# Kernel tuning notes

Measured on AMD Instinct MI355X. Metric: run time of the kernel, lower is better.

## Reference

```python
import jax, jax.numpy as jnp
import numpy as np

N_T = 256
N_LAT = 1024
N_INN = 512
N_G = 512
N_MU = 64
N_NEU = 1024  # MLP hidden width (both MLP_p and MLP_m)
N_HID = 2     # hidden layers per MLP


def _linear(x, w, b=None):
    y = x @ w.T
    return y if b is None else y + b


def _mlp(x, in_w, in_b, h0_w, h0_b, h1_w, h1_b, out_w, out_b):
    f = jax.nn.leaky_relu(_linear(x, in_w, in_b))
    f = jax.nn.leaky_relu(_linear(f, h0_w, h0_b))
    f = jax.nn.leaky_relu(_linear(f, h1_w, h1_b))
    return _linear(f, out_w, out_b)


def setup_inputs() -> dict:
    key = jax.random.key(0)
    ks = jax.random.split(key, 24)

    def w(k, out_f, in_f):
        return jax.random.normal(k, (out_f, in_f), jnp.float32) / np.sqrt(in_f)

    def b(k, out_f):
        return jax.random.normal(k, (out_f,), jnp.float32) * 0.01

    return {
        "mu": jax.random.normal(ks[0], (N_MU,), jnp.float32),
        "z_0": jax.random.normal(ks[1], (N_LAT,), jnp.float32),
        # attention projections (no bias)
        "W1": w(ks[2], N_LAT, N_INN),
        "W2": w(ks[3], N_INN, N_LAT),
        "W3": w(ks[4], N_G, N_LAT),
        # MLP_p: N_MU -> N_NEU -> (x2) -> N_LAT
        "p_in_w": w(ks[5], N_NEU, N_MU), "p_in_b": b(ks[6], N_NEU),
        "p_h0_w": w(ks[7], N_NEU, N_NEU), "p_h0_b": b(ks[8], N_NEU),
        "p_h1_w": w(ks[9], N_NEU, N_NEU), "p_h1_b": b(ks[10], N_NEU),
        "p_out_w": w(ks[11], N_LAT, N_NEU), "p_out_b": b(ks[12], N_LAT),
        # MLP_m: N_G -> N_NEU -> (x2) -> N_LAT
        "m_in_w": w(ks[13], N_NEU, N_G), "m_in_b": b(ks[14], N_NEU),
        "m_h0_w": w(ks[15], N_NEU, N_NEU), "m_h0_b": b(ks[16], N_NEU),
        "m_h1_w": w(ks[17], N_NEU, N_NEU), "m_h1_b": b(ks[18], N_NEU),
        "m_out_w": w(ks[19], N_LAT, N_NEU), "m_out_b": b(ks[20], N_LAT),
    }


def reference(mu, z_0, W1, W2, W3,
              p_in_w, p_in_b, p_h0_w, p_h0_b, p_h1_w, p_h1_b, p_out_w, p_out_b,
              m_in_w, m_in_b, m_h0_w, m_h0_b, m_h1_w, m_h1_b, m_out_w, m_out_b):
    inv_sqrt = 1.0 / jnp.sqrt(jnp.asarray(N_LAT, jnp.float32))

    z_minus = _mlp(mu, p_in_w, p_in_b, p_h0_w, p_h0_b, p_h1_w, p_h1_b, p_out_w, p_out_b)
    Z0 = jnp.zeros((N_T + 1, N_LAT), mu.dtype).at[0].set(z_minus).at[1].set(z_0)

    def step(Z, t):
        # z_prev = Z[t-1]
        z_prev = jax.lax.dynamic_slice(Z, (t - 1, 0), (1, N_LAT))[0]
        # NOTE: faithful to the torch code -- attention over the FULL Z matrix,
        # including not-yet-filled zero rows (they contribute exp(0) to softmax).
        proj = (Z @ W2.T) @ W1.T                      # [N_t+1, N_lat]
        a = jax.nn.softmax(proj @ z_prev * inv_sqrt)  # [N_t+1]
        g = a @ (Z @ W3.T)                            # [N_g]
        z_new = z_prev + _mlp(g, m_in_w, m_in_b, m_h0_w, m_h0_b,
                              m_h1_w, m_h1_b, m_out_w, m_out_b)
        Z = jax.lax.dynamic_update_slice(Z, z_new[None, :], (t, 0))
        return Z, None

    Z_tilde, _ = jax.lax.scan(step, Z0, jnp.arange(2, N_T + 1))
    return Z_tilde
```

## Files before the change

### kernel.cpp

```cpp
#include <hip/hip_runtime.h>
#include <math.h>


#define NTHR 512
#define NBLK 256

#define B_AC  4096
#define B_SM  36864
#define B_C   102400
#define B_D   167936
#define B_E   233472
#define B_ZM  299008
#define B_DCC 364544

typedef int i4 __attribute__((ext_vector_type(4)));

__device__ __forceinline__ float i2f(int x) { return __int_as_float(x); }
__device__ __forceinline__ int f2i(float x) { return __float_as_int(x); }

__device__ __forceinline__ void astore(float* p, float v) {
  __hip_atomic_store(p, v, __ATOMIC_RELAXED, __HIP_MEMORY_SCOPE_AGENT);
}
__device__ __forceinline__ int aloadI(const int* p) {
  return __hip_atomic_load((int*)p, __ATOMIC_RELAXED, __HIP_MEMORY_SCOPE_AGENT);
}
__device__ __forceinline__ int afaddI(int* p) {
  return __hip_atomic_fetch_add(p, 1, __ATOMIC_RELAXED, __HIP_MEMORY_SCOPE_AGENT);
}

__device__ __forceinline__ i4 poll16(const i4* p, int tag) {
  i4 v;
  for (;;) {
    asm volatile("global_load_dwordx4 %0, %1, off sc0 sc1\n\ts_waitcnt vmcnt(0)"
                 : "=&v"(v) : "v"(p) : "memory");
    if (v.w == tag) return v;
    __builtin_amdgcn_s_sleep(1);
  }
}
__device__ __forceinline__ void store16(i4* p, i4 v) {
  asm volatile("global_store_dwordx4 %0, %1, off sc0 sc1" :: "v"(p), "v"(v) : "memory");
}

__device__ __forceinline__ float wred(float v) {
#pragma unroll
  for (int o = 1; o < 64; o <<= 1) v += __shfl_xor(v, o, 64);
  return v;
}
__device__ __forceinline__ void wred2(float& a, float& b) {
#pragma unroll
  for (int o = 1; o < 64; o <<= 1) { a += __shfl_xor(a, o, 64); b += __shfl_xor(b, o, 64); }
}
__device__ __forceinline__ float wmax(float v) {
#pragma unroll
  for (int o = 1; o < 64; o <<= 1) v = fmaxf(v, __shfl_xor(v, o, 64));
  return v;
}
__device__ __forceinline__ float lrelu(float x) { return x > 0.f ? x : 0.01f * x; }

__device__ __forceinline__ void gsync1(int* bar, int bid, int tid, int lane) {
  asm volatile("" ::: "memory");
  __builtin_amdgcn_s_waitcnt(0);
  __syncthreads();
  if (tid == 0) afaddI(bar + (bid & 7) * 16);
  if (tid < 64) {
    for (;;) {
      int v = (lane < 8) ? aloadI(bar + lane * 16) : 0x7fffffff;
      if (__all(v >= 32)) break;
      __builtin_amdgcn_s_sleep(2);
    }
  }
  __syncthreads();
  asm volatile("" ::: "memory");
}

__global__ void __launch_bounds__(NTHR) tcell(
    const float* __restrict__ mu, const float* __restrict__ z0,
    const float* __restrict__ W1, const float* __restrict__ W2, const float* __restrict__ W3,
    const float* __restrict__ p_in_w, const float* __restrict__ p_in_b,
    const float* __restrict__ p_h0_w, const float* __restrict__ p_h0_b,
    const float* __restrict__ p_h1_w, const float* __restrict__ p_h1_b,
    const float* __restrict__ p_out_w, const float* __restrict__ p_out_b,
    const float* __restrict__ m_in_w, const float* __restrict__ m_in_b,
    const float* __restrict__ m_h0_w, const float* __restrict__ m_h0_b,
    const float* __restrict__ m_h1_w, const float* __restrict__ m_h1_b,
    const float* __restrict__ m_out_w, const float* __restrict__ m_out_b,
    float* __restrict__ Z, float* __restrict__ ws) {
  const int tid = threadIdx.x;
  const int bid = blockIdx.x;
  const int lane = tid & 63;
  const int wave = tid >> 6;
  const int r = 4 * bid + (wave & 3);
  const int rep = bid & 7;

  char* wsb = (char*)ws;
  int* bar = (int*)wsb;
  i4* aC  = (i4*)(wsb + B_AC);
  i4* smC = (i4*)(wsb + B_SM);
  i4* cCh = (i4*)(wsb + B_C);
  i4* dCh = (i4*)(wsb + B_D);
  i4* eCh = (i4*)(wsb + B_E);
  i4* zmC = (i4*)(wsb + B_ZM);
  float* dCc = (float*)(wsb + B_DCC);
  i4* aCr  = aC  + rep * 256;
  i4* smCr = smC + rep * 512;
  i4* cChr = cCh + rep * 512;
  i4* dChr = dCh + rep * 512;
  i4* eChr = eCh + rep * 512;
  i4* zmCr = zmC + rep * 512;

  __shared__ float sZ[1024], sX[1024];
  __shared__ float sR[256], sLg[256], sLp[256];
  __shared__ float sU[4][257];
  __shared__ float shW[4], shQ[4], shF[4];

  float4 rB4[4], rW4[4];
  if (wave < 4) {
#pragma unroll
    for (int q = 0; q < 4; ++q) {
      rB4[q] = make_float4(0.f, 0.f, 0.f, 0.f);
      rW4[q] = make_float4(0.f, 0.f, 0.f, 0.f);
    }
    const float* __restrict__ w1r = W1 + (size_t)r * 512;
    const float* __restrict__ mir = m_in_w + (size_t)r * 512;
    for (int k = 0; k < 512; k += 2) {
      float w1a = w1r[k], w1b = w1r[k + 1];
      float mia = mir[k], mib = mir[k + 1];
      const float* w2a = W2 + (size_t)k * 1024 + 4 * lane;
      const float* w3a = W3 + (size_t)k * 1024 + 4 * lane;
#pragma unroll
      for (int q = 0; q < 4; ++q) {
        float4 a0 = *(const float4*)(w2a + 256 * q);
        float4 a1 = *(const float4*)(w2a + 1024 + 256 * q);
        float4 b0 = *(const float4*)(w3a + 256 * q);
        float4 b1 = *(const float4*)(w3a + 1024 + 256 * q);
        rB4[q].x = fmaf(w1a, a0.x, fmaf(w1b, a1.x, rB4[q].x));
        rB4[q].y = fmaf(w1a, a0.y, fmaf(w1b, a1.y, rB4[q].y));
        rB4[q].z = fmaf(w1a, a0.z, fmaf(w1b, a1.z, rB4[q].z));
        rB4[q].w = fmaf(w1a, a0.w, fmaf(w1b, a1.w, rB4[q].w));
        rW4[q].x = fmaf(mia, b0.x, fmaf(mib, b1.x, rW4[q].x));
        rW4[q].y = fmaf(mia, b0.y, fmaf(mib, b1.y, rW4[q].y));
        rW4[q].z = fmaf(mia, b0.z, fmaf(mib, b1.z, rW4[q].z));
        rW4[q].w = fmaf(mia, b0.w, fmaf(mib, b1.w, rW4[q].w));
      }
    }
  } else if (wave == 4) {
    float f[4];
#pragma unroll
    for (int j = 0; j < 4; ++j) {
      int row = 4 * bid + j;
      float acc = p_in_w[(size_t)row * 64 + lane] * mu[lane];
      acc = wred(acc);
      f[j] = lrelu(acc + p_in_b[row]);
    }
    if (lane < 16) {
      int rp = lane >> 1, ch = lane & 1;
      i4 c; c.x = f2i(f[2 * ch]); c.y = f2i(f[2 * ch + 1]); c.z = 0; c.w = 1;
      store16(smC + rp * 512 + 2 * bid + ch, c);
    }
  }

#define MV_PHASE(WPTR, BPTR, ACT, OUTC, TAG)                                   \
  if (wave < 4) {                                                              \
    const float* w = (WPTR) + (size_t)r * 1024 + 4 * lane;                     \
    float acc = 0.f;                                                           \
    _Pragma("unroll")                                                          \
    for (int q = 0; q < 4; ++q) {                                              \
      float4 wf = *(const float4*)(w + 256 * q);                               \
      float4 xf = *(const float4*)(sX + 4 * lane + 256 * q);                   \
      acc = fmaf(wf.x, xf.x, acc); acc = fmaf(wf.y, xf.y, acc);                \
      acc = fmaf(wf.z, xf.z, acc); acc = fmaf(wf.w, xf.w, acc);                \
    }                                                                          \
    acc = wred(acc);                                                           \
    if (lane == 0) shF[wave] = (ACT) ? lrelu(acc + (BPTR)[r]) : (acc + (BPTR)[r]); \
  }                                                                            \
  __syncthreads();                                                             \
  if (tid < 16) {                                                              \
    int rp = tid >> 1, ch = tid & 1;                                           \
    i4 c; c.x = f2i(shF[2 * ch]); c.y = f2i(shF[2 * ch + 1]); c.z = 0; c.w = (TAG); \
    store16((OUTC) + rp * 512 + 2 * bid + ch, c);                              \
  }

  { i4 v = poll16(smCr + tid, 1); sX[2 * tid] = i2f(v.x); sX[2 * tid + 1] = i2f(v.y); }
  __syncthreads();
  MV_PHASE(p_h0_w, p_h0_b, 1, cCh, 1)

  { i4 v = poll16(cChr + tid, 1); sX[2 * tid] = i2f(v.x); sX[2 * tid + 1] = i2f(v.y); }
  __syncthreads();
  MV_PHASE(p_h1_w, p_h1_b, 1, dCh, 1)

  { i4 v = poll16(dChr + tid, 1); sX[2 * tid] = i2f(v.x); sX[2 * tid + 1] = i2f(v.y); }
  __syncthreads();
  MV_PHASE(p_out_w, p_out_b, 0, zmC, 1)
  if (tid == 16) *(float4*)(Z + 4 * bid) = make_float4(shF[0], shF[1], shF[2], shF[3]);
  if (bid < 2) Z[1024 + bid * 512 + tid] = z0[bid * 512 + tid];

  { i4 v = poll16(zmCr + tid, 1); sZ[2 * tid] = i2f(v.x); sZ[2 * tid + 1] = i2f(v.y); }
  __syncthreads();
  if (wave < 4) {
    float aD = 0.f, aU = 0.f;
#pragma unroll
    for (int q = 0; q < 4; ++q) {
      float4 zf = *(const float4*)(sZ + 4 * lane + 256 * q);
      aD = fmaf(rB4[q].x, zf.x, aD); aD = fmaf(rB4[q].y, zf.y, aD);
      aD = fmaf(rB4[q].z, zf.z, aD); aD = fmaf(rB4[q].w, zf.w, aD);
      aU = fmaf(rW4[q].x, zf.x, aU); aU = fmaf(rW4[q].y, zf.y, aU);
      aU = fmaf(rW4[q].z, zf.z, aU); aU = fmaf(rW4[q].w, zf.w, aU);
    }
    wred2(aD, aU);
    if (lane == 0) { astore(dCc + r, aD * 0.03125f); sU[wave][0] = aU; }
  }
  gsync1(bar, bid, tid, lane);

  float zprev_e = 0.f, mob = 0.f;
  if (wave < 4) { zprev_e = z0[r]; mob = m_out_b[r]; }

  for (int t = 2; t <= 256; ++t) {
    if (t == 2) {
      *(float2*)(sZ + 2 * tid) = *(const float2*)(z0 + 2 * tid);
    } else {
      i4 v = poll16(eChr + tid, t - 1);
      sZ[2 * tid] = i2f(v.x); sZ[2 * tid + 1] = i2f(v.y);
    }
    __syncthreads();
    if (wave < 4) {
      float aD = 0.f, aU = 0.f;
#pragma unroll
      for (int q = 0; q < 4; ++q) {
        float4 zf = *(const float4*)(sZ + 4 * lane + 256 * q);
        aD = fmaf(rB4[q].x, zf.x, aD); aD = fmaf(rB4[q].y, zf.y, aD);
        aD = fmaf(rB4[q].z, zf.z, aD); aD = fmaf(rB4[q].w, zf.w, aD);
        aU = fmaf(rW4[q].x, zf.x, aU); aU = fmaf(rW4[q].y, zf.y, aU);
        aU = fmaf(rW4[q].z, zf.z, aU); aU = fmaf(rW4[q].w, zf.w, aU);
      }
      wred2(aD, aU);
      if (lane == 0) {
        float dsc = aD * 0.03125f;
        astore(dCc + (size_t)(t - 1) * 1024 + r, dsc);
        sU[wave][t - 1] = aU;
        shW[wave] = dsc * sZ[r];
      }
    } else {
      float part = 0.f;
      if (bid <= t - 2) {
        const float* dr = dCc + (size_t)bid * 1024 + 256 * (wave - 4) + 4 * lane;
        float4 d4 = *(const float4*)dr;
        const float* zz = sZ + 256 * (wave - 4) + 4 * lane;
        part = d4.x * zz[0] + d4.y * zz[1] + d4.z * zz[2] + d4.w * zz[3];
      }
      part = wred(part);
      if (lane == 0) shQ[wave - 4] = part;
    }
    __builtin_amdgcn_s_waitcnt(0);
    __syncthreads();
    if (tid < 8) {
      i4 c; c.x = f2i(shQ[0] + shQ[1] + shQ[2] + shQ[3]);
      c.y = f2i(shW[0] + shW[1] + shW[2] + shW[3]); c.z = 0; c.w = t;
      store16(aC + tid * 256 + bid, c);
    }

    if (tid < 256) {
      i4 v = poll16(aCr + tid, t);
      sLg[tid] = i2f(v.x); sLp[tid] = i2f(v.y);
    }
    __syncthreads();
    if (wave == 0) {
      float p = sLp[lane] + sLp[lane + 64] + sLp[lane + 128] + sLp[lane + 192];
      p = wred(p);
      float l[4]; float mx = -1e30f;
#pragma unroll
      for (int j = 0; j < 4; ++j) {
        int i = lane + 64 * j;
        float li = (i <= t - 2) ? sLg[i] : ((i == t - 1) ? p : -1e30f);
        l[j] = li; mx = fmaxf(mx, li);
      }
      mx = wmax(mx);
      float m = fmaxf(mx, 0.f);
      float e[4], es = 0.f;
#pragma unroll
      for (int j = 0; j < 4; ++j) {
        int i = lane + 64 * j;
        e[j] = (i <= t - 1) ? __expf(l[j] - m) : 0.f;
        es += e[j];
      }
      es = wred(es);
      float inv = 1.f / (es + (float)(257 - t) * __expf(-m));
#pragma unroll
      for (int j = 0; j < 4; ++j) sR[lane + 64 * j] = e[j] * inv;
    }
    __syncthreads();
    if (wave < 4) {
      float acc = 0.f;
#pragma unroll
      for (int j = 0; j < 4; ++j) {
        int i = lane + 64 * j;
        if (i <= t - 1) acc = fmaf(sR[i], sU[wave][i], acc);
      }
      acc = wred(acc);
      if (lane == 0) shF[wave] = lrelu(acc + m_in_b[r]);
    }
    __syncthreads();
    if (tid < 16) {
      int rp = tid >> 1, ch = tid & 1;
      i4 c; c.x = f2i(shF[2 * ch]); c.y = f2i(shF[2 * ch + 1]); c.z = 0; c.w = t;
      store16(smC + rp * 512 + 2 * bid + ch, c);
    }

    { i4 v = poll16(smCr + tid, t); sX[2 * tid] = i2f(v.x); sX[2 * tid + 1] = i2f(v.y); }
    __syncthreads();
    MV_PHASE(m_h0_w, m_h0_b, 1, cCh, t)

    { i4 v = poll16(cChr + tid, t); sX[2 * tid] = i2f(v.x); sX[2 * tid + 1] = i2f(v.y); }
    __syncthreads();
    MV_PHASE(m_h1_w, m_h1_b, 1, dCh, t)

    { i4 v = poll16(dChr + tid, t); sX[2 * tid] = i2f(v.x); sX[2 * tid + 1] = i2f(v.y); }
    __syncthreads();
    if (wave < 4) {
      const float* w = m_out_w + (size_t)r * 1024 + 4 * lane;
      float acc = 0.f;
#pragma unroll
      for (int q = 0; q < 4; ++q) {
        float4 wf = *(const float4*)(w + 256 * q);
        float4 xf = *(const float4*)(sX + 4 * lane + 256 * q);
        acc = fmaf(wf.x, xf.x, acc); acc = fmaf(wf.y, xf.y, acc);
        acc = fmaf(wf.z, xf.z, acc); acc = fmaf(wf.w, xf.w, acc);
      }
      acc = wred(acc);
      float znew = zprev_e + acc + mob;
      zprev_e = znew;
      if (lane == 0) shF[wave] = znew;
    }
    __syncthreads();
    if (tid < 16) {
      int rp = tid >> 1, ch = tid & 1;
      i4 c; c.x = f2i(shF[2 * ch]); c.y = f2i(shF[2 * ch + 1]); c.z = 0; c.w = t;
      store16(eCh + rp * 512 + 2 * bid + ch, c);
    }
    if (tid == 16)
      *(float4*)(Z + (size_t)t * 1024 + 4 * bid) =
          make_float4(shF[0], shF[1], shF[2], shF[3]);
  }
}

extern "C" void kernel_launch(void* const* d_in, const int* in_sizes, int n_in,
                              void* d_out, int out_size, void* d_ws, size_t ws_size,
                              hipStream_t stream) {
  (void)in_sizes; (void)n_in; (void)out_size; (void)ws_size;
  hipMemsetAsync(d_ws, 0, 364544, stream);
  tcell<<<dim3(NBLK), dim3(NTHR), 0, stream>>>(
      (const float*)d_in[0],  (const float*)d_in[1],
      (const float*)d_in[2],  (const float*)d_in[3],  (const float*)d_in[4],
      (const float*)d_in[5],  (const float*)d_in[6],
      (const float*)d_in[7],  (const float*)d_in[8],
      (const float*)d_in[9],  (const float*)d_in[10],
      (const float*)d_in[11], (const float*)d_in[12],
      (const float*)d_in[13], (const float*)d_in[14],
      (const float*)d_in[15], (const float*)d_in[16],
      (const float*)d_in[17], (const float*)d_in[18],
      (const float*)d_in[19], (const float*)d_in[20],
      (float*)d_out, (float*)d_ws);
}
```

Measured before the change: 3.298 ms.

## Poll cross-block chunks with a single wave and prefetch weights before waiting

Every thread in every block used to spin on its own tagged 16-byte chunk. Now one wave (wave 7) polls all chunks, issuing several loads per lane, and writes the values to shared memory before the block barrier. The matvec weight rows are also loaded into registers before the poll, so their global-memory latency overlaps the wait for the previous layer. The aim is less polling traffic on the coherence point and less per-phase latency in this latency-bound persistent kernel. In exchange, a single wave now serialises the gather, and the weights stay in registers longer, raising register pressure.

After: 4.262 ms. 29.3% more time.

```diff
diff --git a/kernel.cpp b/kernel.cpp
--- a/kernel.cpp
+++ b/kernel.cpp
@@ -28,17 +28,54 @@
   return __hip_atomic_fetch_add(p, 1, __ATOMIC_RELAXED, __HIP_MEMORY_SCOPE_AGENT);
 }
 
-__device__ __forceinline__ i4 poll16(const i4* p, int tag) {
-  i4 v;
-  for (;;) {
-    asm volatile("global_load_dwordx4 %0, %1, off sc0 sc1\n\ts_waitcnt vmcnt(0)"
-                 : "=&v"(v) : "v"(p) : "memory");
-    if (v.w == tag) return v;
-    __builtin_amdgcn_s_sleep(1);
-  }
-}
 __device__ __forceinline__ void store16(i4* p, i4 v) {
   asm volatile("global_store_dwordx4 %0, %1, off sc0 sc1" :: "v"(p), "v"(v) : "memory");
+}
+
+template<int CPL>
+__device__ __forceinline__ void wpoll(const i4* base, int tag, int lane, float* dst) {
+  i4 v[CPL];
+  int got = 0;
+  const int full = (1 << CPL) - 1;
+  for (;;) {
+#pragma unroll
+    for (int k = 0; k < CPL; ++k)
+      if (!(got & (1 << k)))
+        asm volatile("global_load_dwordx4 %0, %1, off sc0 sc1"
+                     : "=v"(v[k]) : "v"(base + CPL * lane + k) : "memory");
+    asm volatile("s_waitcnt vmcnt(0)" ::: "memory");
+#pragma unroll
+    for (int k = 0; k < CPL; ++k)
+      if (!(got & (1 << k)) && v[k].w == tag) {
+        got |= 1 << k;
+        dst[2 * (CPL * lane + k)] = i2f(v[k].x);
+        dst[2 * (CPL * lane + k) + 1] = i2f(v[k].y);
+      }
+    if (__all(got == full)) return;
+    __builtin_amdgcn_s_sleep(1);
+  }
+}
+__device__ __forceinline__ void wpoll2(const i4* base, int tag, int lane,
+                                       float* dA, float* dB) {
+  i4 v[4];
+  int got = 0;
+  for (;;) {
+#pragma unroll
+    for (int k = 0; k < 4; ++k)
+      if (!(got & (1 << k)))
+        asm volatile("global_load_dwordx4 %0, %1, off sc0 sc1"
+                     : "=v"(v[k]) : "v"(base + 4 * lane + k) : "memory");
+    asm volatile("s_waitcnt vmcnt(0)" ::: "memory");
+#pragma unroll
+    for (int k = 0; k < 4; ++k)
+      if (!(got & (1 << k)) && v[k].w == tag) {
+        got |= 1 << k;
+        dA[4 * lane + k] = i2f(v[k].x);
+        dB[4 * lane + k] = i2f(v[k].y);
+      }
+    if (__all(got == 15)) return;
+    __builtin_amdgcn_s_sleep(1);
+  }
 }
 
 __device__ __forceinline__ float wred(float v) {
@@ -159,42 +196,46 @@
     }
   }
 
-#define MV_PHASE(WPTR, BPTR, ACT, OUTC, TAG)                                   \
-  if (wave < 4) {                                                              \
-    const float* w = (WPTR) + (size_t)r * 1024 + 4 * lane;                     \
-    float acc = 0.f;                                                           \
-    _Pragma("unroll")                                                          \
-    for (int q = 0; q < 4; ++q) {                                              \
-      float4 wf = *(const float4*)(w + 256 * q);                               \
-      float4 xf = *(const float4*)(sX + 4 * lane + 256 * q);                   \
-      acc = fmaf(wf.x, xf.x, acc); acc = fmaf(wf.y, xf.y, acc);                \
-      acc = fmaf(wf.z, xf.z, acc); acc = fmaf(wf.w, xf.w, acc);                \
+#define MVP(WPTR, BPTR, ACT, INC, INTAG, OUTC, OUTTAG)                         \
+  {                                                                            \
+    float4 wreg[4];                                                            \
+    if (wave < 4) {                                                            \
+      const float* w = (WPTR) + (size_t)r * 1024 + 4 * lane;                   \
+      _Pragma("unroll")                                                        \
+      for (int q = 0; q < 4; ++q) wreg[q] = *(const float4*)(w + 256 * q);     \
     }                                                                          \
-    acc = wred(acc);                                                           \
-    if (lane == 0) shF[wave] = (ACT) ? lrelu(acc + (BPTR)[r]) : (acc + (BPTR)[r]); \
-  }                                                                            \
-  __syncthreads();                                                             \
-  if (tid < 16) {                                                              \
-    int rp = tid >> 1, ch = tid & 1;                                           \
-    i4 c; c.x = f2i(shF[2 * ch]); c.y = f2i(shF[2 * ch + 1]); c.z = 0; c.w = (TAG); \
-    store16((OUTC) + rp * 512 + 2 * bid + ch, c);                              \
-  }
-
-  { i4 v = poll16(smCr + tid, 1); sX[2 * tid] = i2f(v.x); sX[2 * tid + 1] = i2f(v.y); }
-  __syncthreads();
-  MV_PHASE(p_h0_w, p_h0_b, 1, cCh, 1)
-
-  { i4 v = poll16(cChr + tid, 1); sX[2 * tid] = i2f(v.x); sX[2 * tid + 1] = i2f(v.y); }
-  __syncthreads();
-  MV_PHASE(p_h1_w, p_h1_b, 1, dCh, 1)
-
-  { i4 v = poll16(dChr + tid, 1); sX[2 * tid] = i2f(v.x); sX[2 * tid + 1] = i2f(v.y); }
-  __syncthreads();
-  MV_PHASE(p_out_w, p_out_b, 0, zmC, 1)
+    if (wave == 7) wpoll<8>((INC), (INTAG), lane, sX);                         \
+    __syncthreads();                                                           \
+    if (wave < 4) {                                                            \
+      float acc = 0.f;                                                         \
+      _Pragma("unroll")                                                        \
+      for (int q = 0; q < 4; ++q) {                                            \
+        float4 xf = *(const float4*)(sX + 4 * lane + 256 * q);                 \
+        acc = fmaf(wreg[q].x, xf.x, acc); acc = fmaf(wreg[q].y, xf.y, acc);    \
+        acc = fmaf(wreg[q].z, xf.z, acc); acc = fmaf(wreg[q].w, xf.w, acc);    \
+      }                                                                        \
+      acc = wred(acc);                                                         \
+      if (lane == 0) {                                                         \
+        float vv = acc + (BPTR)[r];                                            \
+        shF[wave] = (ACT) ? lrelu(vv) : vv;                                    \
+      }                                                                        \
+    }                                                                          \
+    __syncthreads();                                                           \
+    if (tid < 16) {                                                            \
+      int rp = tid >> 1, ch = tid & 1;                                         \
+      i4 c; c.x = f2i(shF[2 * ch]); c.y = f2i(shF[2 * ch + 1]); c.z = 0;       \
+      c.w = (OUTTAG);                                                          \
+      store16((OUTC) + rp * 512 + 2 * bid + ch, c);                            \
+    }                                                                          \
+  }
+
+  MVP(p_h0_w, p_h0_b, 1, smCr, 1, cCh, 1)
+  MVP(p_h1_w, p_h1_b, 1, cChr, 1, dCh, 1)
+  MVP(p_out_w, p_out_b, 0, dChr, 1, zmC, 1)
   if (tid == 16) *(float4*)(Z + 4 * bid) = make_float4(shF[0], shF[1], shF[2], shF[3]);
   if (bid < 2) Z[1024 + bid * 512 + tid] = z0[bid * 512 + tid];
 
-  { i4 v = poll16(zmCr + tid, 1); sZ[2 * tid] = i2f(v.x); sZ[2 * tid + 1] = i2f(v.y); }
+  if (wave == 7) wpoll<8>(zmCr, 1, lane, sZ);
   __syncthreads();
   if (wave < 4) {
     float aD = 0.f, aU = 0.f;
@@ -218,8 +259,7 @@
     if (t == 2) {
       *(float2*)(sZ + 2 * tid) = *(const float2*)(z0 + 2 * tid);
     } else {
-      i4 v = poll16(eChr + tid, t - 1);
-      sZ[2 * tid] = i2f(v.x); sZ[2 * tid + 1] = i2f(v.y);
+      if (wave == 7) wpoll<8>(eChr, t - 1, lane, sZ);
     }
     __syncthreads();
     if (wave < 4) {
@@ -258,10 +298,7 @@
       store16(aC + tid * 256 + bid, c);
     }
 
-    if (tid < 256) {
-      i4 v = poll16(aCr + tid, t);
-      sLg[tid] = i2f(v.x); sLp[tid] = i2f(v.y);
-    }
+    if (wave == 7) wpoll2(aCr, t, lane, sLg, sLp);
     __syncthreads();
     if (wave == 0) {
       float p = sLp[lane] + sLp[lane + 64] + sLp[lane + 128] + sLp[lane + 192];
@@ -305,40 +342,42 @@
       store16(smC + rp * 512 + 2 * bid + ch, c);
     }
 
-    { i4 v = poll16(smCr + tid, t); sX[2 * tid] = i2f(v.x); sX[2 * tid + 1] = i2f(v.y); }
-    __syncthreads();
-    MV_PHASE(m_h0_w, m_h0_b, 1, cCh, t)
-
-    { i4 v = poll16(cChr + tid, t); sX[2 * tid] = i2f(v.x); sX[2 * tid + 1] = i2f(v.y); }
-    __syncthreads();
-    MV_PHASE(m_h1_w, m_h1_b, 1, dCh, t)
-
-    { i4 v = poll16(dChr + tid, t); sX[2 * tid] = i2f(v.x); sX[2 * tid + 1] = i2f(v.y); }
-    __syncthreads();
-    if (wave < 4) {
-      const float* w = m_out_w + (size_t)r * 1024 + 4 * lane;
-      float acc = 0.f;
-#pragma unroll
-      for (int q = 0; q < 4; ++q) {
-        float4 wf = *(const float4*)(w + 256 * q);
-        float4 xf = *(const float4*)(sX + 4 * lane + 256 * q);
-        acc = fmaf(wf.x, xf.x, acc); acc = fmaf(wf.y, xf.y, acc);
-        acc = fmaf(wf.z, xf.z, acc); acc = fmaf(wf.w, xf.w, acc);
-      }
-      acc = wred(acc);
-      float znew = zprev_e + acc + mob;
-      zprev_e = znew;
-      if (lane == 0) shF[wave] = znew;
-    }
-    __syncthreads();
-    if (tid < 16) {
-      int rp = tid >> 1, ch = tid & 1;
-      i4 c; c.x = f2i(shF[2 * ch]); c.y = f2i(shF[2 * ch + 1]); c.z = 0; c.w = t;
-      store16(eCh + rp * 512 + 2 * bid + ch, c);
-    }
-    if (tid == 16)
-      *(float4*)(Z + (size_t)t * 1024 + 4 * bid) =
-          make_float4(shF[0], shF[1], shF[2], shF[3]);
+    MVP(m_h0_w, m_h0_b, 1, smCr, t, cCh, t)
+
+    MVP(m_h1_w, m_h1_b, 1, cChr, t, dCh, t)
+
+    {
+      float4 wreg[4];
+      if (wave < 4) {
+        const float* w = m_out_w + (size_t)r * 1024 + 4 * lane;
+#pragma unroll
+        for (int q = 0; q < 4; ++q) wreg[q] = *(const float4*)(w + 256 * q);
+      }
+      if (wave == 7) wpoll<8>(dChr, t, lane, sX);
+      __syncthreads();
+      if (wave < 4) {
+        float acc = 0.f;
+#pragma unroll
+        for (int q = 0; q < 4; ++q) {
+          float4 xf = *(const float4*)(sX + 4 * lane + 256 * q);
+          acc = fmaf(wreg[q].x, xf.x, acc); acc = fmaf(wreg[q].y, xf.y, acc);
+          acc = fmaf(wreg[q].z, xf.z, acc); acc = fmaf(wreg[q].w, xf.w, acc);
+        }
+        acc = wred(acc);
+        float znew = zprev_e + acc + mob;
+        zprev_e = znew;
+        if (lane == 0) shF[wave] = znew;
+      }
+      __syncthreads();
+      if (tid < 16) {
+        int rp = tid >> 1, ch = tid & 1;
+        i4 c; c.x = f2i(shF[2 * ch]); c.y = f2i(shF[2 * ch + 1]); c.z = 0; c.w = t;
+        store16(eCh + rp * 512 + 2 * bid + ch, c);
+      }
+      if (tid == 16)
+        *(float4*)(Z + (size_t)t * 1024 + 4 * bid) =
+            make_float4(shF[0], shF[1], shF[2], shF[3]);
+    }
   }
 }
 
```

## Fold m_out projection into attention matrices to remove one global sync stage per step

Applied to the files above, without the earlier changes.

Precomputes per-row products of the combined attention projection vectors with m_out_w, so the score and key updates for a new timestep come directly from the last MLP hidden layer instead of waiting for the output layer to produce z_new. The per-step chain of cross-block handoffs loses one stage: the output layer merges into the attention update, and the logit contributions are maintained incrementally using a pipelined g-vector exchange. In exchange it adds a large one-time setup (a 1024x1024 sweep per wave), more shared memory, and much more complex bookkeeping, with some risk of floating-point drift from the reassociated sums.

New measurement: 4.533 ms. 1.37x slower.

```diff
diff --git a/kernel.cpp b/kernel.cpp
--- a/kernel.cpp
+++ b/kernel.cpp
@@ -5,13 +5,13 @@
 #define NTHR 512
 #define NBLK 256
 
-#define B_AC  4096
-#define B_SM  36864
-#define B_C   102400
-#define B_D   167936
-#define B_E   233472
-#define B_ZM  299008
-#define B_DCC 364544
+#define B_AC   4096
+#define B_SM   36864
+#define B_C    102400
+#define B_F    167936
+#define B_ZM   233472
+#define B_GC   299008
+#define B_DV   315392
 
 typedef int i4 __attribute__((ext_vector_type(4)));
 
@@ -20,6 +20,10 @@
 
 __device__ __forceinline__ void astore(float* p, float v) {
   __hip_atomic_store(p, v, __ATOMIC_RELAXED, __HIP_MEMORY_SCOPE_AGENT);
+}
+__device__ __forceinline__ float2 aload2(const float* p) {
+  double d = __hip_atomic_load((double*)p, __ATOMIC_RELAXED, __HIP_MEMORY_SCOPE_AGENT);
+  return __builtin_bit_cast(float2, d);
 }
 __device__ __forceinline__ int aloadI(const int* p) {
   return __hip_atomic_load((int*)p, __ATOMIC_RELAXED, __HIP_MEMORY_SCOPE_AGENT);
@@ -49,6 +53,12 @@
 __device__ __forceinline__ void wred2(float& a, float& b) {
 #pragma unroll
   for (int o = 1; o < 64; o <<= 1) { a += __shfl_xor(a, o, 64); b += __shfl_xor(b, o, 64); }
+}
+__device__ __forceinline__ void wred3(float& a, float& b, float& c) {
+#pragma unroll
+  for (int o = 1; o < 64; o <<= 1) {
+    a += __shfl_xor(a, o, 64); b += __shfl_xor(b, o, 64); c += __shfl_xor(c, o, 64);
+  }
 }
 __device__ __forceinline__ float wmax(float v) {
 #pragma unroll
@@ -97,21 +107,21 @@
   i4* aC  = (i4*)(wsb + B_AC);
   i4* smC = (i4*)(wsb + B_SM);
   i4* cCh = (i4*)(wsb + B_C);
-  i4* dCh = (i4*)(wsb + B_D);
-  i4* eCh = (i4*)(wsb + B_E);
+  i4* fCh = (i4*)(wsb + B_F);
   i4* zmC = (i4*)(wsb + B_ZM);
-  float* dCc = (float*)(wsb + B_DCC);
+  i4* gC  = (i4*)(wsb + B_GC);
+  float* dVec = (float*)(wsb + B_DV);
   i4* aCr  = aC  + rep * 256;
   i4* smCr = smC + rep * 512;
   i4* cChr = cCh + rep * 512;
-  i4* dChr = dCh + rep * 512;
-  i4* eChr = eCh + rep * 512;
+  i4* fChr = fCh + rep * 512;
   i4* zmCr = zmC + rep * 512;
 
-  __shared__ float sZ[1024], sX[1024];
-  __shared__ float sR[256], sLg[256], sLp[256];
+  __shared__ float sX[1024], sDv[1024];
+  __shared__ float sLg[256], sNp[256], sPp[256], sR[256];
+  __shared__ float sBigB[4][1024], sBigW[4][1024];
   __shared__ float sU[4][257];
-  __shared__ float shW[4], shQ[4], shF[4];
+  __shared__ float shD[4], shDp[4], shZ[4], shG[4], shGv[4], shF[4];
 
   float4 rB4[4], rW4[4];
   if (wave < 4) {
@@ -159,7 +169,9 @@
     }
   }
 
-#define MV_PHASE(WPTR, BPTR, ACT, OUTC, TAG)                                   \
+#define MVP(WPTR, BPTR, ACT, INC, INTAG, OUTC, OUTTAG)                         \
+  { i4 v = poll16((INC) + tid, (INTAG)); sX[2*tid] = i2f(v.x); sX[2*tid+1] = i2f(v.y); } \
+  __syncthreads();                                                             \
   if (wave < 4) {                                                              \
     const float* w = (WPTR) + (size_t)r * 1024 + 4 * lane;                     \
     float acc = 0.f;                                                           \
@@ -171,106 +183,184 @@
       acc = fmaf(wf.z, xf.z, acc); acc = fmaf(wf.w, xf.w, acc);                \
     }                                                                          \
     acc = wred(acc);                                                           \
-    if (lane == 0) shF[wave] = (ACT) ? lrelu(acc + (BPTR)[r]) : (acc + (BPTR)[r]); \
+    if (lane == 0) { float vv = acc + (BPTR)[r]; shF[wave] = (ACT) ? lrelu(vv) : vv; } \
   }                                                                            \
   __syncthreads();                                                             \
   if (tid < 16) {                                                              \
     int rp = tid >> 1, ch = tid & 1;                                           \
-    i4 c; c.x = f2i(shF[2 * ch]); c.y = f2i(shF[2 * ch + 1]); c.z = 0; c.w = (TAG); \
+    i4 c; c.x = f2i(shF[2*ch]); c.y = f2i(shF[2*ch+1]); c.z = 0; c.w = (OUTTAG); \
     store16((OUTC) + rp * 512 + 2 * bid + ch, c);                              \
   }
 
-  { i4 v = poll16(smCr + tid, 1); sX[2 * tid] = i2f(v.x); sX[2 * tid + 1] = i2f(v.y); }
-  __syncthreads();
-  MV_PHASE(p_h0_w, p_h0_b, 1, cCh, 1)
-
-  { i4 v = poll16(cChr + tid, 1); sX[2 * tid] = i2f(v.x); sX[2 * tid + 1] = i2f(v.y); }
-  __syncthreads();
-  MV_PHASE(p_h1_w, p_h1_b, 1, dCh, 1)
-
-  { i4 v = poll16(dChr + tid, 1); sX[2 * tid] = i2f(v.x); sX[2 * tid + 1] = i2f(v.y); }
-  __syncthreads();
-  MV_PHASE(p_out_w, p_out_b, 0, zmC, 1)
+  MVP(p_h0_w, p_h0_b, 1, smCr, 1, cCh, 1)
+  MVP(p_h1_w, p_h1_b, 1, cChr, 1, fCh, 1)
+  MVP(p_out_w, p_out_b, 0, fChr, 1, zmC, 1)
   if (tid == 16) *(float4*)(Z + 4 * bid) = make_float4(shF[0], shF[1], shF[2], shF[3]);
   if (bid < 2) Z[1024 + bid * 512 + tid] = z0[bid * 512 + tid];
 
-  { i4 v = poll16(zmCr + tid, 1); sZ[2 * tid] = i2f(v.x); sZ[2 * tid + 1] = i2f(v.y); }
+  float d0_w = 0.f, d_prev = 0.f, z_prev = 0.f;
+  { i4 v = poll16(zmCr + tid, 1); sDv[2*tid] = i2f(v.x); sDv[2*tid+1] = i2f(v.y); }
+  { float2 a = *(const float2*)(z0 + 2 * tid); sX[2*tid] = a.x; sX[2*tid+1] = a.y; }
   __syncthreads();
   if (wave < 4) {
-    float aD = 0.f, aU = 0.f;
+    float aD = 0.f, aU = 0.f, bD = 0.f, bU = 0.f;
 #pragma unroll
     for (int q = 0; q < 4; ++q) {
-      float4 zf = *(const float4*)(sZ + 4 * lane + 256 * q);
-      aD = fmaf(rB4[q].x, zf.x, aD); aD = fmaf(rB4[q].y, zf.y, aD);
-      aD = fmaf(rB4[q].z, zf.z, aD); aD = fmaf(rB4[q].w, zf.w, aD);
-      aU = fmaf(rW4[q].x, zf.x, aU); aU = fmaf(rW4[q].y, zf.y, aU);
-      aU = fmaf(rW4[q].z, zf.z, aU); aU = fmaf(rW4[q].w, zf.w, aU);
-    }
-    wred2(aD, aU);
-    if (lane == 0) { astore(dCc + r, aD * 0.03125f); sU[wave][0] = aU; }
+      float4 zm = *(const float4*)(sDv + 4 * lane + 256 * q);
+      float4 z1 = *(const float4*)(sX + 4 * lane + 256 * q);
+      aD = fmaf(rB4[q].x, zm.x, aD); aD = fmaf(rB4[q].y, zm.y, aD);
+      aD = fmaf(rB4[q].z, zm.z, aD); aD = fmaf(rB4[q].w, zm.w, aD);
+      aU = fmaf(rW4[q].x, zm.x, aU); aU = fmaf(rW4[q].y, zm.y, aU);
+      aU = fmaf(rW4[q].z, zm.z, aU); aU = fmaf(rW4[q].w, zm.w, aU);
+      bD = fmaf(rB4[q].x, z1.x, bD); bD = fmaf(rB4[q].y, z1.y, bD);
+      bD = fmaf(rB4[q].z, z1.z, bD); bD = fmaf(rB4[q].w, z1.w, bD);
+      bU = fmaf(rW4[q].x, z1.x, bU); bU = fmaf(rW4[q].y, z1.y, bU);
+      bU = fmaf(rW4[q].z, z1.z, bU); bU = fmaf(rW4[q].w, z1.w, bU);
+    }
+    wred2(aD, aU); wred2(bD, bU);
+    d0_w = aD; d_prev = bD; z_prev = z0[r];
+    if (lane == 0) {
+      sU[wave][0] = aU; sU[wave][1] = bU;
+      astore(dVec + 1024 + r, aD);
+      astore(dVec + r, bD);
+    }
   }
   gsync1(bar, bid, tid, lane);
 
-  float zprev_e = 0.f, mob = 0.f;
-  if (wave < 4) { zprev_e = z0[r]; mob = m_out_b[r]; }
+  float lgreg = 0.f, dmob = 0.f;
+  float4 G4 = make_float4(0.f, 0.f, 0.f, 0.f);
+
+#define GWORK(PAR, TAG, ROWID)                                                 \
+  { float2 a = aload2(dVec + (PAR) * 1024 + 2 * tid);                          \
+    sDv[2*tid] = a.x; sDv[2*tid+1] = a.y; }                                    \
+  __syncthreads();                                                             \
+  if (wave < 4) {                                                              \
+    int j = 4 * bid + wave;                                                    \
+    float acc = 0.f;                                                           \
+    _Pragma("unroll")                                                          \
+    for (int jj = 0; jj < 16; ++jj)                                            \
+      acc = fmaf(m_out_w[(size_t)(lane + 64*jj) * 1024 + j], sDv[lane + 64*jj], acc); \
+    acc = wred(acc);                                                           \
+    if (lane == 0) shGv[wave] = acc;                                           \
+  }                                                                            \
+  { float pd = sDv[tid] * m_out_b[tid] + sDv[tid+512] * m_out_b[tid+512];      \
+    sX[tid] = pd; }                                                            \
+  __syncthreads();                                                             \
+  if (wave == 0) {                                                             \
+    float s = sX[lane] + sX[lane+64] + sX[lane+128] + sX[lane+192]             \
+            + sX[lane+256] + sX[lane+320] + sX[lane+384] + sX[lane+448];       \
+    s = wred(s);                                                               \
+    if (bid == (ROWID)) dmob = s;                                              \
+    if (lane < 2) {                                                            \
+      i4 c; c.x = f2i(shGv[2*lane]); c.y = f2i(shGv[2*lane+1]); c.z = 0;       \
+      c.w = (TAG);                                                             \
+      store16(gC + (PAR) * 512 + 2 * bid + lane, c);                           \
+    }                                                                          \
+  }
+
+  GWORK(1, 1, 0)
+
+  float4 rBM[4], rWM[4], rMo[4];
+  float bmob = 0.f, wmob = 0.f, mob_own = 0.f;
+  if (wave < 4) {
+#pragma unroll
+    for (int q = 0; q < 4; ++q) {
+      *(float4*)(&sBigB[wave][4 * lane + 256 * q]) = rB4[q];
+      *(float4*)(&sBigW[wave][4 * lane + 256 * q]) = rW4[q];
+      rBM[q] = make_float4(0.f, 0.f, 0.f, 0.f);
+      rWM[q] = make_float4(0.f, 0.f, 0.f, 0.f);
+    }
+  }
+  __syncthreads();
+  if (wave < 4) {
+    for (int m = 0; m < 1024; ++m) {
+      float bB = sBigB[wave][m], bW = sBigW[wave][m];
+      float mb = m_out_b[m];
+      bmob = fmaf(bB, mb, bmob); wmob = fmaf(bW, mb, wmob);
+      const float* mo = m_out_w + (size_t)m * 1024 + 4 * lane;
+#pragma unroll
+      for (int q = 0; q < 4; ++q) {
+        float4 m4 = *(const float4*)(mo + 256 * q);
+        rBM[q].x = fmaf(bB, m4.x, rBM[q].x); rBM[q].y = fmaf(bB, m4.y, rBM[q].y);
+        rBM[q].z = fmaf(bB, m4.z, rBM[q].z); rBM[q].w = fmaf(bB, m4.w, rBM[q].w);
+        rWM[q].x = fmaf(bW, m4.x, rWM[q].x); rWM[q].y = fmaf(bW, m4.y, rWM[q].y);
+        rWM[q].z = fmaf(bW, m4.z, rWM[q].z); rWM[q].w = fmaf(bW, m4.w, rWM[q].w);
+      }
+    }
+#pragma unroll
+    for (int q = 0; q < 4; ++q)
+      rMo[q] = *(const float4*)(m_out_w + (size_t)r * 1024 + 4 * lane + 256 * q);
+    mob_own = m_out_b[r];
+  }
 
   for (int t = 2; t <= 256; ++t) {
     if (t == 2) {
-      *(float2*)(sZ + 2 * tid) = *(const float2*)(z0 + 2 * tid);
+      if (wave < 4 && lane == 0) { shD[wave] = d_prev; shDp[wave] = d0_w; shZ[wave] = z_prev; }
+      __syncthreads();
     } else {
-      i4 v = poll16(eChr + tid, t - 1);
-      sZ[2 * tid] = i2f(v.x); sZ[2 * tid + 1] = i2f(v.y);
-    }
-    __syncthreads();
-    if (wave < 4) {
-      float aD = 0.f, aU = 0.f;
-#pragma unroll
-      for (int q = 0; q < 4; ++q) {
-        float4 zf = *(const float4*)(sZ + 4 * lane + 256 * q);
-        aD = fmaf(rB4[q].x, zf.x, aD); aD = fmaf(rB4[q].y, zf.y, aD);
-        aD = fmaf(rB4[q].z, zf.z, aD); aD = fmaf(rB4[q].w, zf.w, aD);
-        aU = fmaf(rW4[q].x, zf.x, aU); aU = fmaf(rW4[q].y, zf.y, aU);
-        aU = fmaf(rW4[q].z, zf.z, aU); aU = fmaf(rW4[q].w, zf.w, aU);
-      }
-      wred2(aD, aU);
-      if (lane == 0) {
-        float dsc = aD * 0.03125f;
-        astore(dCc + (size_t)(t - 1) * 1024 + r, dsc);
-        sU[wave][t - 1] = aU;
-        shW[wave] = dsc * sZ[r];
-      }
-    } else {
-      float part = 0.f;
-      if (bid <= t - 2) {
-        const float* dr = dCc + (size_t)bid * 1024 + 256 * (wave - 4) + 4 * lane;
-        float4 d4 = *(const float4*)dr;
-        const float* zz = sZ + 256 * (wave - 4) + 4 * lane;
-        part = d4.x * zz[0] + d4.y * zz[1] + d4.z * zz[2] + d4.w * zz[3];
-      }
-      part = wred(part);
-      if (lane == 0) shQ[wave - 4] = part;
-    }
-    __builtin_amdgcn_s_waitcnt(0);
-    __syncthreads();
-    if (tid < 8) {
-      i4 c; c.x = f2i(shQ[0] + shQ[1] + shQ[2] + shQ[3]);
-      c.y = f2i(shW[0] + shW[1] + shW[2] + shW[3]); c.z = 0; c.w = t;
-      store16(aC + tid * 256 + bid, c);
+      { i4 v = poll16(fChr + tid, t - 1); sX[2*tid] = i2f(v.x); sX[2*tid+1] = i2f(v.y); }
+      __syncthreads();
+      if (wave < 4) {
+        float dB = 0.f, dW = 0.f, dM = 0.f;
+#pragma unroll
+        for (int q = 0; q < 4; ++q) {
+          float4 xf = *(const float4*)(sX + 4 * lane + 256 * q);
+          dB = fmaf(rBM[q].x, xf.x, dB); dB = fmaf(rBM[q].y, xf.y, dB);
+          dB = fmaf(rBM[q].z, xf.z, dB); dB = fmaf(rBM[q].w, xf.w, dB);
+          dW = fmaf(rWM[q].x, xf.x, dW); dW = fmaf(rWM[q].y, xf.y, dW);
+          dW = fmaf(rWM[q].z, xf.z, dW); dW = fmaf(rWM[q].w, xf.w, dW);
+          dM = fmaf(rMo[q].x, xf.x, dM); dM = fmaf(rMo[q].y, xf.y, dM);
+          dM = fmaf(rMo[q].z, xf.z, dM); dM = fmaf(rMo[q].w, xf.w, dM);
+        }
+        wred3(dB, dW, dM);
+        float d_new = d_prev + dB + bmob;
+        float U_new = sU[wave][t - 2] + dW + wmob;
+        float z_new = z_prev + dM + mob_own;
+        if (lane == 0) {
+          sU[wave][t - 1] = U_new;
+          astore(Z + (size_t)(t - 1) * 1024 + r, z_new);
+          astore(dVec + (t & 1) * 1024 + r, d_new);
+          shD[wave] = d_new; shDp[wave] = d_prev; shZ[wave] = z_new;
+        }
+        __builtin_amdgcn_s_waitcnt(0);
+        d_prev = d_new; z_prev = z_new;
+      } else {
+        int u = tid - 256;
+        float gp = G4.x * sX[4*u] + G4.y * sX[4*u+1] + G4.z * sX[4*u+2] + G4.w * sX[4*u+3];
+        gp = wred(gp);
+        if (lane == 0) shG[wave - 4] = gp;
+      }
+      __syncthreads();
+    }
+    if (wave == 0) {
+      float np = shD[0]*shZ[0] + shD[1]*shZ[1] + shD[2]*shZ[2] + shD[3]*shZ[3];
+      float pp = shDp[0]*shZ[0] + shDp[1]*shZ[1] + shDp[2]*shZ[2] + shDp[3]*shZ[3];
+      if (t >= 3 && bid <= t - 3)
+        lgreg += shG[0] + shG[1] + shG[2] + shG[3] + dmob;
+      if (lane < 8) {
+        i4 c; c.x = f2i(lgreg); c.y = f2i(np); c.z = f2i(pp); c.w = t;
+        store16(aC + lane * 256 + bid, c);
+      }
     }
 
     if (tid < 256) {
       i4 v = poll16(aCr + tid, t);
-      sLg[tid] = i2f(v.x); sLp[tid] = i2f(v.y);
+      sLg[tid] = i2f(v.x); sNp[tid] = i2f(v.y); sPp[tid] = i2f(v.z);
     }
     __syncthreads();
     if (wave == 0) {
-      float p = sLp[lane] + sLp[lane + 64] + sLp[lane + 128] + sLp[lane + 192];
-      p = wred(p);
+      float ns = sNp[lane] + sNp[lane+64] + sNp[lane+128] + sNp[lane+192];
+      float ps = sPp[lane] + sPp[lane+64] + sPp[lane+128] + sPp[lane+192];
+      wred2(ns, ps);
+      if (bid == t - 2) lgreg = ps;
       float l[4]; float mx = -1e30f;
 #pragma unroll
       for (int j = 0; j < 4; ++j) {
         int i = lane + 64 * j;
-        float li = (i <= t - 2) ? sLg[i] : ((i == t - 1) ? p : -1e30f);
+        float li = -1e30f;
+        if (i <= t - 3) li = sLg[i] * 0.03125f;
+        else if (i == t - 2) li = ps * 0.03125f;
+        else if (i == t - 1) li = ns * 0.03125f;
         l[j] = li; mx = fmaxf(mx, li);
       }
       mx = wmax(mx);
@@ -301,44 +391,40 @@
     __syncthreads();
     if (tid < 16) {
       int rp = tid >> 1, ch = tid & 1;
-      i4 c; c.x = f2i(shF[2 * ch]); c.y = f2i(shF[2 * ch + 1]); c.z = 0; c.w = t;
+      i4 c; c.x = f2i(shF[2*ch]); c.y = f2i(shF[2*ch+1]); c.z = 0; c.w = t;
       store16(smC + rp * 512 + 2 * bid + ch, c);
     }
 
-    { i4 v = poll16(smCr + tid, t); sX[2 * tid] = i2f(v.x); sX[2 * tid + 1] = i2f(v.y); }
-    __syncthreads();
-    MV_PHASE(m_h0_w, m_h0_b, 1, cCh, t)
-
-    { i4 v = poll16(cChr + tid, t); sX[2 * tid] = i2f(v.x); sX[2 * tid + 1] = i2f(v.y); }
-    __syncthreads();
-    MV_PHASE(m_h1_w, m_h1_b, 1, dCh, t)
-
-    { i4 v = poll16(dChr + tid, t); sX[2 * tid] = i2f(v.x); sX[2 * tid + 1] = i2f(v.y); }
-    __syncthreads();
-    if (wave < 4) {
-      const float* w = m_out_w + (size_t)r * 1024 + 4 * lane;
-      float acc = 0.f;
-#pragma unroll
-      for (int q = 0; q < 4; ++q) {
-        float4 wf = *(const float4*)(w + 256 * q);
-        float4 xf = *(const float4*)(sX + 4 * lane + 256 * q);
-        acc = fmaf(wf.x, xf.x, acc); acc = fmaf(wf.y, xf.y, acc);
-        acc = fmaf(wf.z, xf.z, acc); acc = fmaf(wf.w, xf.w, acc);
-      }
-      acc = wred(acc);
-      float znew = zprev_e + acc + mob;
-      zprev_e = znew;
-      if (lane == 0) shF[wave] = znew;
-    }
-    __syncthreads();
-    if (tid < 16) {
-      int rp = tid >> 1, ch = tid & 1;
-      i4 c; c.x = f2i(shF[2 * ch]); c.y = f2i(shF[2 * ch + 1]); c.z = 0; c.w = t;
-      store16(eCh + rp * 512 + 2 * bid + ch, c);
-    }
-    if (tid == 16)
-      *(float4*)(Z + (size_t)t * 1024 + 4 * bid) =
-          make_float4(shF[0], shF[1], shF[2], shF[3]);
+    MVP(m_h0_w, m_h0_b, 1, smCr, t, cCh, t)
+
+    MVP(m_h1_w, m_h1_b, 1, cChr, t, fCh, t)
+
+    if (t <= 254) {
+      GWORK((t & 1), t, t - 1)
+    }
+    if (t == bid + 2 && bid <= 253) {
+      if (tid >= 256) {
+        int u = tid - 256;
+        const i4* gbase = gC + ((bid + 1) & 1) * 512;
+        i4 c0 = poll16(gbase + 2 * u, bid + 1);
+        i4 c1 = poll16(gbase + 2 * u + 1, bid + 1);
+        G4.x = i2f(c0.x); G4.y = i2f(c0.y); G4.z = i2f(c1.x); G4.w = i2f(c1.y);
+      }
+    }
+  }
+
+  { i4 v = poll16(fChr + tid, 256); sX[2*tid] = i2f(v.x); sX[2*tid+1] = i2f(v.y); }
+  __syncthreads();
+  if (wave < 4) {
+    float dM = 0.f;
+#pragma unroll
+    for (int q = 0; q < 4; ++q) {
+      float4 xf = *(const float4*)(sX + 4 * lane + 256 * q);
+      dM = fmaf(rMo[q].x, xf.x, dM); dM = fmaf(rMo[q].y, xf.y, dM);
+      dM = fmaf(rMo[q].z, xf.z, dM); dM = fmaf(rMo[q].w, xf.w, dM);
+    }
+    dM = wred(dM);
+    if (lane == 0) astore(Z + (size_t)256 * 1024 + r, z_prev + dM + mob_own);
   }
 }
 
@@ -346,7 +432,7 @@
                               void* d_out, int out_size, void* d_ws, size_t ws_size,
                               hipStream_t stream) {
   (void)in_sizes; (void)n_in; (void)out_size; (void)ws_size;
-  hipMemsetAsync(d_ws, 0, 364544, stream);
+  hipMemsetAsync(d_ws, 0, 315392, stream);
   tcell<<<dim3(NBLK), dim3(NTHR), 0, stream>>>(
       (const float*)d_in[0],  (const float*)d_in[1],
       (const float*)d_in[2],  (const float*)d_in[3],  (const float*)d_in[4],
```
